# Optimization experiments

Measured on AMD Instinct MI355X. Metric: run time of the kernel, lower is better.

## Reference

```python
import jax, jax.numpy as jnp
import numpy as np

N_A, N_B, N_C = 100000, 60000, 40000
N = N_A + N_B + N_C  # 200000 total nodes after concat
E = 3200000
D_IN = (512, 256, 128)
D = 64  # com_feat_dim == emb_dim


def setup_inputs() -> dict:
    key = jax.random.key(0)
    ks = jax.random.split(key, 16)
    inp = {
        "feat_a": jax.random.normal(ks[0], (N_A, D_IN[0]), jnp.float32),
        "W_a": jax.random.normal(ks[1], (D_IN[0], D), jnp.float32) * 0.05,
        "b_a": jax.random.normal(ks[2], (D,), jnp.float32) * 0.05,
        "feat_b": jax.random.normal(ks[3], (N_B, D_IN[1]), jnp.float32),
        "W_b": jax.random.normal(ks[4], (D_IN[1], D), jnp.float32) * 0.05,
        "b_b": jax.random.normal(ks[5], (D,), jnp.float32) * 0.05,
        "feat_c": jax.random.normal(ks[6], (N_C, D_IN[2]), jnp.float32),
        "W_c": jax.random.normal(ks[7], (D_IN[2], D), jnp.float32) * 0.05,
        "b_c": jax.random.normal(ks[8], (D,), jnp.float32) * 0.05,
        "gcn_W": jax.random.normal(ks[9], (D, D), jnp.float32) * 0.1,
        "gcn_b": jax.random.normal(ks[10], (D,), jnp.float32) * 0.05,
        "edge_weight": jax.random.uniform(ks[11], (E,), jnp.float32),
        "edge_src": jax.random.randint(ks[12], (E,), 0, N, jnp.int32),
        "edge_dst": jax.random.randint(ks[13], (E,), 0, N, jnp.int32),
    }
    return inp


def reference(feat_a, W_a, b_a, feat_b, W_b, b_b, feat_c, W_c, b_c,
              gcn_W, gcn_b, edge_weight, edge_src, edge_dst):
    # Per-type linear encoders + ReLU, then concat over the node axis
    enc = jnp.concatenate([
        jax.nn.relu(feat_a @ W_a + b_a),
        jax.nn.relu(feat_b @ W_b + b_b),
        jax.nn.relu(feat_c @ W_c + b_c),
    ], axis=0)  # [N, D]
    # GraphConvolution: out = spmm(adj, enc @ W + b)
    support = enc @ gcn_W + gcn_b                    # [N, D]
    msg = support[edge_src] * edge_weight[:, None]   # [E, D] irregular gather
    com_emb = jax.ops.segment_sum(msg, edge_dst, num_segments=N)  # [N, D]
    # F.normalize(p=2, dim=1)
    norm = jnp.linalg.norm(com_emb, axis=1, keepdims=True)
    com_emb = com_emb / jnp.maximum(norm, 1e-12)
    return com_emb
```

## Files before the change

kernel.cpp:

```cpp
#include <hip/hip_runtime.h>

#define N_A 100000
#define N_B 60000
#define N_C 40000
#define NTOT 200000
#define NEDGE 3200000
#define D 64

#define SCAN_BLK 1024
#define NB_SCAN ((NTOT + SCAN_BLK - 1) / SCAN_BLK)

__device__ __forceinline__ void tile_mm64(const float* __restrict__ sA,
                                          const float* __restrict__ sW,
                                          const int nidx[4], int d0,
                                          float acc[4][2])
{
#pragma unroll
    for (int kk = 0; kk < 64; kk += 4) {
        float wl[4], wh[4];
#pragma unroll
        for (int u = 0; u < 4; ++u) {
            wl[u] = sW[(kk + u) * 64 + d0];
            wh[u] = sW[(kk + u) * 64 + d0 + 32];
        }
#pragma unroll
        for (int j = 0; j < 4; ++j) {
            const float4 f = *(const float4*)(sA + nidx[j] * 64 + kk);
            acc[j][0] = fmaf(f.x, wl[0], acc[j][0]);
            acc[j][0] = fmaf(f.y, wl[1], acc[j][0]);
            acc[j][0] = fmaf(f.z, wl[2], acc[j][0]);
            acc[j][0] = fmaf(f.w, wl[3], acc[j][0]);
            acc[j][1] = fmaf(f.x, wh[0], acc[j][1]);
            acc[j][1] = fmaf(f.y, wh[1], acc[j][1]);
            acc[j][1] = fmaf(f.z, wh[2], acc[j][1]);
            acc[j][1] = fmaf(f.w, wh[3], acc[j][1]);
        }
    }
}

template <int K>
__global__ __launch_bounds__(256) void enc_gcn_kernel(
    const float* __restrict__ feat, const float* __restrict__ W,
    const float* __restrict__ bias, const float* __restrict__ gW,
    const float* __restrict__ gb, float* __restrict__ support, int node0)
{
    __shared__ float sW[64 * 64];
    __shared__ float sF[32 * 64];
    __shared__ float sE[32 * 64];

    const int tid = threadIdx.x;
    const int d0  = tid & 31;
    const int h   = (tid >> 5) & 1;
    const int w   = tid >> 6;
    const int blockNode = blockIdx.x * 32;

    int nidx[4];
#pragma unroll
    for (int j = 0; j < 4; ++j) nidx[j] = j * 8 + w * 2 + h;

    float acc[4][2] = {};

    for (int k0 = 0; k0 < K; k0 += 64) {
#pragma unroll
        for (int i = 0; i < 16; ++i) {
            int idx = i * 256 + tid;
            sW[idx] = W[(long long)(k0 + (idx >> 6)) * 64 + (idx & 63)];
        }
#pragma unroll
        for (int i = 0; i < 8; ++i) {
            int idx = i * 256 + tid;
            sF[idx] = feat[(long long)(blockNode + (idx >> 6)) * K + k0 + (idx & 63)];
        }
        __syncthreads();
        tile_mm64(sF, sW, nidx, d0, acc);
        __syncthreads();
    }

    {
        const float b0 = bias[d0], b1 = bias[d0 + 32];
#pragma unroll
        for (int j = 0; j < 4; ++j) {
            sE[nidx[j] * 64 + d0]      = fmaxf(acc[j][0] + b0, 0.f);
            sE[nidx[j] * 64 + d0 + 32] = fmaxf(acc[j][1] + b1, 0.f);
        }
    }
#pragma unroll
    for (int i = 0; i < 16; ++i) {
        int idx = i * 256 + tid;
        sW[idx] = gW[idx];
    }
    __syncthreads();

    float a2[4][2] = {};
    tile_mm64(sE, sW, nidx, d0, a2);

    const float g0 = gb[d0], g1 = gb[d0 + 32];
#pragma unroll
    for (int j = 0; j < 4; ++j) {
        const long long row = (long long)(node0 + blockNode + nidx[j]);
        support[row * 64 + d0]      = a2[j][0] + g0;
        support[row * 64 + d0 + 32] = a2[j][1] + g1;
    }
}

__global__ void zero_ints(int* __restrict__ p, int n)
{
    int i = blockIdx.x * blockDim.x + threadIdx.x;
    if (i < n) p[i] = 0;
}

__global__ void hist_kernel(const int* __restrict__ edst, int* __restrict__ deg, int e)
{
    int i  = blockIdx.x * blockDim.x + threadIdx.x;
    int st = gridDim.x * blockDim.x;
    for (; i < e; i += st) atomicAdd(&deg[edst[i]], 1);
}

__global__ __launch_bounds__(SCAN_BLK) void s1_blocksums(const int* __restrict__ deg,
                                                         int* __restrict__ partials, int n)
{
    const int tid = threadIdx.x;
    const int i   = blockIdx.x * SCAN_BLK + tid;
    int v = (i < n) ? deg[i] : 0;
#pragma unroll
    for (int o = 32; o; o >>= 1) v += __shfl_xor(v, o, 64);
    __shared__ int wsum[SCAN_BLK / 64];
    if ((tid & 63) == 0) wsum[tid >> 6] = v;
    __syncthreads();
    if (tid == 0) {
        int s = 0;
#pragma unroll
        for (int w = 0; w < SCAN_BLK / 64; ++w) s += wsum[w];
        partials[blockIdx.x] = s;
    }
}

__global__ __launch_bounds__(256) void s2_scan(const int* __restrict__ partials,
                                               int* __restrict__ pscan, int np)
{
    __shared__ int arr[512];
    if (threadIdx.x < np) arr[threadIdx.x] = partials[threadIdx.x];
    __syncthreads();
    if (threadIdx.x == 0) {
        int run = 0;
        for (int i = 0; i < np; ++i) { int t = arr[i]; arr[i] = run; run += t; }
    }
    __syncthreads();
    if (threadIdx.x < np) pscan[threadIdx.x] = arr[threadIdx.x];
}

__global__ __launch_bounds__(SCAN_BLK) void s3_scan(const int* __restrict__ deg,
                                                    const int* __restrict__ pscan,
                                                    int* __restrict__ row_start,
                                                    int* __restrict__ cursor, int n)
{
    const int tid  = threadIdx.x;
    const int lane = tid & 63, wid = tid >> 6;
    const int i    = blockIdx.x * SCAN_BLK + tid;
    int v = (i < n) ? deg[i] : 0;
    int x = v;
#pragma unroll
    for (int o = 1; o < 64; o <<= 1) {
        int y = __shfl_up(x, o, 64);
        if (lane >= o) x += y;
    }
    __shared__ int wsum[SCAN_BLK / 64];
    if (lane == 63) wsum[wid] = x;
    __syncthreads();
    if (tid == 0) {
        int run = 0;
#pragma unroll
        for (int w = 0; w < SCAN_BLK / 64; ++w) { int t = wsum[w]; wsum[w] = run; run += t; }
    }
    __syncthreads();
    if (i < n) {
        const int excl = x - v + wsum[wid] + pscan[blockIdx.x];
        row_start[i] = excl;
        cursor[i]    = excl;
    }
}

__global__ void fill_kernel(const int* __restrict__ esrc, const int* __restrict__ edst,
                            const float* __restrict__ ew, int* __restrict__ cursor,
                            uint2* __restrict__ csr, int e)
{
    int i  = blockIdx.x * blockDim.x + threadIdx.x;
    int st = gridDim.x * blockDim.x;
    for (; i < e; i += st) {
        const int t   = edst[i];
        const int pos = atomicAdd(&cursor[t], 1);
        csr[pos] = make_uint2((unsigned)esrc[i], __float_as_uint(ew[i]));
    }
}

__global__ __launch_bounds__(256) void gather_norm_kernel(const float* __restrict__ support,
                                                          const uint2* __restrict__ csr,
                                                          const int* __restrict__ row_start,
                                                          const int* __restrict__ deg,
                                                          float* __restrict__ out)
{
    const int lane = threadIdx.x & 63;
    const int nid  = blockIdx.x * 4 + (threadIdx.x >> 6);
    if (nid >= NTOT) return;
    const int base = row_start[nid];
    const int dg   = deg[nid];

    float acc = 0.f;
    int i = 0;
    for (; i + 4 <= dg; i += 4) {
        const uint2 c0 = csr[base + i + 0];
        const uint2 c1 = csr[base + i + 1];
        const uint2 c2 = csr[base + i + 2];
        const uint2 c3 = csr[base + i + 3];
        const float v0 = support[(long long)c0.x * D + lane];
        const float v1 = support[(long long)c1.x * D + lane];
        const float v2 = support[(long long)c2.x * D + lane];
        const float v3 = support[(long long)c3.x * D + lane];
        acc = fmaf(v0, __uint_as_float(c0.y), acc);
        acc = fmaf(v1, __uint_as_float(c1.y), acc);
        acc = fmaf(v2, __uint_as_float(c2.y), acc);
        acc = fmaf(v3, __uint_as_float(c3.y), acc);
    }
    for (; i < dg; ++i) {
        const uint2 c = csr[base + i];
        acc = fmaf(support[(long long)c.x * D + lane], __uint_as_float(c.y), acc);
    }

    float ss = acc * acc;
#pragma unroll
    for (int o = 32; o; o >>= 1) ss += __shfl_xor(ss, o, 64);
    const float nrm = fmaxf(sqrtf(ss), 1e-12f);
    out[(long long)nid * D + lane] = acc / nrm;
}

__global__ void zero_kernel(float4* __restrict__ p, long long n4)
{
    long long i  = (long long)blockIdx.x * blockDim.x + threadIdx.x;
    long long st = (long long)gridDim.x * blockDim.x;
    for (; i < n4; i += st) p[i] = float4{0.f, 0.f, 0.f, 0.f};
}

__global__ void scatter_kernel(const float* __restrict__ support,
                               const float* __restrict__ ew,
                               const int* __restrict__ esrc,
                               const int* __restrict__ edst,
                               float* __restrict__ out, int E)
{
    const int d  = threadIdx.x & 63;
    int gw       = blockIdx.x * (blockDim.x >> 6) + (threadIdx.x >> 6);
    const int nw = gridDim.x * (blockDim.x >> 6);
    for (int e = gw; e < E; e += nw) {
        const int   s  = esrc[e];
        const int   t  = edst[e];
        const float we = ew[e];
        atomicAdd(&out[(long long)t * 64 + d], support[(long long)s * 64 + d] * we);
    }
}

__global__ void normalize_kernel(float* __restrict__ out, int N)
{
    const int d   = threadIdx.x & 63;
    const int row = blockIdx.x * (blockDim.x >> 6) + (threadIdx.x >> 6);
    if (row < N) {
        const long long base = (long long)row * 64;
        float x  = out[base + d];
        float ss = x * x;
#pragma unroll
        for (int o = 32; o; o >>= 1) ss += __shfl_xor(ss, o, 64);
        const float nrm = fmaxf(sqrtf(ss), 1e-12f);
        out[base + d] = x / nrm;
    }
}

extern "C" void kernel_launch(void* const* d_in, const int* in_sizes, int n_in,
                              void* d_out, int out_size, void* d_ws, size_t ws_size,
                              hipStream_t stream)
{
    const float* feat_a = (const float*)d_in[0];
    const float* W_a    = (const float*)d_in[1];
    const float* b_a    = (const float*)d_in[2];
    const float* feat_b = (const float*)d_in[3];
    const float* W_b    = (const float*)d_in[4];
    const float* b_b    = (const float*)d_in[5];
    const float* feat_c = (const float*)d_in[6];
    const float* W_c    = (const float*)d_in[7];
    const float* b_c    = (const float*)d_in[8];
    const float* gcn_W  = (const float*)d_in[9];
    const float* gcn_b  = (const float*)d_in[10];
    const float* ew     = (const float*)d_in[11];
    const int*   esrc   = (const int*)d_in[12];
    const int*   edst   = (const int*)d_in[13];

    float* out = (float*)d_out;

    char* ws = (char*)d_ws;
    const size_t off_support = 0;
    const size_t off_deg     = off_support + (size_t)NTOT * D * 4;
    const size_t off_rowst   = off_deg   + (size_t)NTOT * 4;
    const size_t off_cursor  = off_rowst + (size_t)NTOT * 4;
    const size_t off_part    = off_cursor + (size_t)NTOT * 4;
    const size_t off_pscan   = off_part  + 1024;
    const size_t off_csr     = off_pscan + 1024;
    const size_t need        = off_csr + (size_t)NEDGE * 8;

    float* support = (float*)(ws + off_support);

    enc_gcn_kernel<512><<<N_A / 32, 256, 0, stream>>>(feat_a, W_a, b_a, gcn_W, gcn_b, support, 0);
    enc_gcn_kernel<256><<<N_B / 32, 256, 0, stream>>>(feat_b, W_b, b_b, gcn_W, gcn_b, support, N_A);
    enc_gcn_kernel<128><<<N_C / 32, 256, 0, stream>>>(feat_c, W_c, b_c, gcn_W, gcn_b, support, N_A + N_B);

    if (ws_size >= need) {
        int*   deg     = (int*)(ws + off_deg);
        int*   rowst   = (int*)(ws + off_rowst);
        int*   cursor  = (int*)(ws + off_cursor);
        int*   part    = (int*)(ws + off_part);
        int*   pscan   = (int*)(ws + off_pscan);
        uint2* csr     = (uint2*)(ws + off_csr);

        zero_ints<<<(NTOT + 255) / 256, 256, 0, stream>>>(deg, NTOT);
        hist_kernel<<<4096, 256, 0, stream>>>(edst, deg, NEDGE);
        s1_blocksums<<<NB_SCAN, SCAN_BLK, 0, stream>>>(deg, part, NTOT);
        s2_scan<<<1, 256, 0, stream>>>(part, pscan, NB_SCAN);
        s3_scan<<<NB_SCAN, SCAN_BLK, 0, stream>>>(deg, pscan, rowst, cursor, NTOT);
        fill_kernel<<<4096, 256, 0, stream>>>(esrc, edst, ew, cursor, csr, NEDGE);

        gather_norm_kernel<<<(NTOT + 3) / 4, 256, 0, stream>>>(support, csr, rowst, deg, out);
    } else {
        zero_kernel<<<2048, 256, 0, stream>>>((float4*)out, (long long)NTOT * D / 4);
        scatter_kernel<<<8192, 256, 0, stream>>>(support, ew, esrc, edst, out, NEDGE);
        normalize_kernel<<<NTOT / 4, 256, 0, stream>>>(out, NTOT);
    }
}
```

Measured before the change: 1.042 ms.

## Replace fused encoder+GCN kernel with register-tiled 256-node GEMM kernels

Replaces the 32-node-per-block fused encoder/GCN-weight kernel with a generic 8x8 register-tiled GEMM kernel handling 256 nodes per block, with K-major shared-memory feature tiles and float4 loads and stores. The second matmul (gcn_W) is unfused into a separate launch, with the encoder output staged in the output buffer. The aim is higher FMA-to-load ratio and far less per-block weight reloading. In exchange it adds an extra 51MB round trip through global memory and one more launch, and uses more registers per thread.

```diff
diff --git a/kernel.cpp b/kernel.cpp
--- a/kernel.cpp
+++ b/kernel.cpp
@@ -10,96 +10,85 @@
 #define SCAN_BLK 1024
 #define NB_SCAN ((NTOT + SCAN_BLK - 1) / SCAN_BLK)
 
-__device__ __forceinline__ void tile_mm64(const float* __restrict__ sA,
-                                          const float* __restrict__ sW,
-                                          const int nidx[4], int d0,
-                                          float acc[4][2])
-{
-#pragma unroll
-    for (int kk = 0; kk < 64; kk += 4) {
-        float wl[4], wh[4];
-#pragma unroll
-        for (int u = 0; u < 4; ++u) {
-            wl[u] = sW[(kk + u) * 64 + d0];
-            wh[u] = sW[(kk + u) * 64 + d0 + 32];
+template <int K, bool RELU>
+__global__ __launch_bounds__(256) void gemm64_kernel(
+    const float* __restrict__ X, const float* __restrict__ W,
+    const float* __restrict__ bias, float* __restrict__ Y,
+    int Nn, int node0out)
+{
+    __shared__ float sF[32][260];
+    __shared__ float sW[32 * 64];
+
+    const int tid = threadIdx.x;
+    const int td  = tid & 7;
+    const int tn  = tid >> 3;
+    const int d0  = td * 8;
+    const int n0  = tn * 8;
+    const int blockNode = blockIdx.x * 256;
+
+    float acc[8][8] = {};
+
+    for (int k0 = 0; k0 < K; k0 += 32) {
+        {
+            const float4* gw = (const float4*)(W + (long long)k0 * 64);
+#pragma unroll
+            for (int i = 0; i < 2; ++i) {
+                const int idx = i * 256 + tid;
+                ((float4*)sW)[idx] = gw[idx];
+            }
         }
-#pragma unroll
-        for (int j = 0; j < 4; ++j) {
-            const float4 f = *(const float4*)(sA + nidx[j] * 64 + kk);
-            acc[j][0] = fmaf(f.x, wl[0], acc[j][0]);
-            acc[j][0] = fmaf(f.y, wl[1], acc[j][0]);
-            acc[j][0] = fmaf(f.z, wl[2], acc[j][0]);
-            acc[j][0] = fmaf(f.w, wl[3], acc[j][0]);
-            acc[j][1] = fmaf(f.x, wh[0], acc[j][1]);
-            acc[j][1] = fmaf(f.y, wh[1], acc[j][1]);
-            acc[j][1] = fmaf(f.z, wh[2], acc[j][1]);
-            acc[j][1] = fmaf(f.w, wh[3], acc[j][1]);
-        }
-    }
-}
-
-template <int K>
-__global__ __launch_bounds__(256) void enc_gcn_kernel(
-    const float* __restrict__ feat, const float* __restrict__ W,
-    const float* __restrict__ bias, const float* __restrict__ gW,
-    const float* __restrict__ gb, float* __restrict__ support, int node0)
-{
-    __shared__ float sW[64 * 64];
-    __shared__ float sF[32 * 64];
-    __shared__ float sE[32 * 64];
-
-    const int tid = threadIdx.x;
-    const int d0  = tid & 31;
-    const int h   = (tid >> 5) & 1;
-    const int w   = tid >> 6;
-    const int blockNode = blockIdx.x * 32;
-
-    int nidx[4];
-#pragma unroll
-    for (int j = 0; j < 4; ++j) nidx[j] = j * 8 + w * 2 + h;
-
-    float acc[4][2] = {};
-
-    for (int k0 = 0; k0 < K; k0 += 64) {
-#pragma unroll
-        for (int i = 0; i < 16; ++i) {
-            int idx = i * 256 + tid;
-            sW[idx] = W[(long long)(k0 + (idx >> 6)) * 64 + (idx & 63)];
-        }
-#pragma unroll
-        for (int i = 0; i < 8; ++i) {
-            int idx = i * 256 + tid;
-            sF[idx] = feat[(long long)(blockNode + (idx >> 6)) * K + k0 + (idx & 63)];
+        {
+            const int tk = tid & 7;
+            const int nl = tid >> 3;
+#pragma unroll
+            for (int p = 0; p < 8; ++p) {
+                const int n  = p * 32 + nl;
+                const int gn = blockNode + n;
+                float4 f = make_float4(0.f, 0.f, 0.f, 0.f);
+                if (gn < Nn)
+                    f = *(const float4*)(X + (long long)gn * K + k0 + tk * 4);
+                sF[tk * 4 + 0][n] = f.x;
+                sF[tk * 4 + 1][n] = f.y;
+                sF[tk * 4 + 2][n] = f.z;
+                sF[tk * 4 + 3][n] = f.w;
+            }
         }
         __syncthreads();
-        tile_mm64(sF, sW, nidx, d0, acc);
+
+#pragma unroll 4
+        for (int kk = 0; kk < 32; ++kk) {
+            const float4 w0 = *(const float4*)(sW + kk * 64 + d0);
+            const float4 w1 = *(const float4*)(sW + kk * 64 + d0 + 4);
+            const float4 f0 = *(const float4*)(&sF[kk][n0]);
+            const float4 f1 = *(const float4*)(&sF[kk][n0 + 4]);
+            float wv[8] = { w0.x, w0.y, w0.z, w0.w, w1.x, w1.y, w1.z, w1.w };
+            float fv[8] = { f0.x, f0.y, f0.z, f0.w, f1.x, f1.y, f1.z, f1.w };
+#pragma unroll
+            for (int j = 0; j < 8; ++j)
+#pragma unroll
+                for (int i = 0; i < 8; ++i)
+                    acc[j][i] = fmaf(fv[j], wv[i], acc[j][i]);
+        }
         __syncthreads();
     }
 
-    {
-        const float b0 = bias[d0], b1 = bias[d0 + 32];
-#pragma unroll
-        for (int j = 0; j < 4; ++j) {
-            sE[nidx[j] * 64 + d0]      = fmaxf(acc[j][0] + b0, 0.f);
-            sE[nidx[j] * 64 + d0 + 32] = fmaxf(acc[j][1] + b1, 0.f);
+    float bv[8];
+    *(float4*)&bv[0] = *(const float4*)(bias + d0);
+    *(float4*)&bv[4] = *(const float4*)(bias + d0 + 4);
+#pragma unroll
+    for (int j = 0; j < 8; ++j) {
+        const int gn = blockNode + n0 + j;
+        if (gn < Nn) {
+            float o[8];
+#pragma unroll
+            for (int i = 0; i < 8; ++i) {
+                o[i] = acc[j][i] + bv[i];
+                if (RELU) o[i] = fmaxf(o[i], 0.f);
+            }
+            float* yp = Y + (long long)(node0out + gn) * 64 + d0;
+            *(float4*)(yp)     = *(float4*)&o[0];
+            *(float4*)(yp + 4) = *(float4*)&o[4];
         }
-    }
-#pragma unroll
-    for (int i = 0; i < 16; ++i) {
-        int idx = i * 256 + tid;
-        sW[idx] = gW[idx];
-    }
-    __syncthreads();
-
-    float a2[4][2] = {};
-    tile_mm64(sE, sW, nidx, d0, a2);
-
-    const float g0 = gb[d0], g1 = gb[d0 + 32];
-#pragma unroll
-    for (int j = 0; j < 4; ++j) {
-        const long long row = (long long)(node0 + blockNode + nidx[j]);
-        support[row * 64 + d0]      = a2[j][0] + g0;
-        support[row * 64 + d0 + 32] = a2[j][1] + g1;
     }
 }
 
@@ -305,9 +294,10 @@
 
     float* support = (float*)(ws + off_support);
 
-    enc_gcn_kernel<512><<<N_A / 32, 256, 0, stream>>>(feat_a, W_a, b_a, gcn_W, gcn_b, support, 0);
-    enc_gcn_kernel<256><<<N_B / 32, 256, 0, stream>>>(feat_b, W_b, b_b, gcn_W, gcn_b, support, N_A);
-    enc_gcn_kernel<128><<<N_C / 32, 256, 0, stream>>>(feat_c, W_c, b_c, gcn_W, gcn_b, support, N_A + N_B);
+    gemm64_kernel<512, true ><<<(N_A  + 255) / 256, 256, 0, stream>>>(feat_a, W_a, b_a, out, N_A, 0);
+    gemm64_kernel<256, true ><<<(N_B  + 255) / 256, 256, 0, stream>>>(feat_b, W_b, b_b, out, N_B, N_A);
+    gemm64_kernel<128, true ><<<(N_C  + 255) / 256, 256, 0, stream>>>(feat_c, W_c, b_c, out, N_C, N_A + N_B);
+    gemm64_kernel< 64, false><<<(NTOT + 255) / 256, 256, 0, stream>>>(out, gcn_W, gcn_b, support, NTOT, 0);
 
     if (ws_size >= need) {
         int*   deg     = (int*)(ws + off_deg);
```

Result: slower. 1.112 ms (+6.7%).
